# Optimization experiments

Hardware: AMD Instinct MI355X
Metric: run time of the kernel (lower is better)

The kernel has to match this reference:

```python
import jax, jax.numpy as jnp
import numpy as np
from jax import lax

C_DIM = 64
N_HEADS = 8
PATCH = 3
PAD = (PATCH - 1) // 2
EPS = 1e-6


def _unfold(x, p, pad):
    # x: [B,C,H,W] -> [B, C*p*p, H*W], torch.F.unfold ordering (C slowest, then ph, pw)
    B, C, H, W = x.shape
    xp = jnp.pad(x, ((0, 0), (0, 0), (pad, pad), (pad, pad)))
    cols = jnp.stack([xp[:, :, i:i + H, j:j + W] for i in range(p) for j in range(p)], axis=2)
    return cols.reshape(B, C * p * p, H * W)


def _fold(cols, p, pad, H, W):
    # cols: [B, C*p*p, H*W] -> [B,C,H,W] via col2im scatter-add (torch.F.fold)
    B = cols.shape[0]
    C = cols.shape[1] // (p * p)
    cols = cols.reshape(B, C, p * p, H, W)
    out = jnp.zeros((B, C, H + 2 * pad, W + 2 * pad), cols.dtype)
    for i in range(p):
        for j in range(p):
            out = out.at[:, :, i:i + H, j:j + W].add(cols[:, :, i * p + j])
    return out[:, :, pad:pad + H, pad:pad + W]


def _linear_attn(q, k, v):
    # q,k,v: [B, h, N, d]; non-softmax linear attention with ReLU features
    kv = jnp.einsum('bhnd,bhne->bhde', k, v)          # [B,h,d,d]
    ksum = k.sum(axis=2)                              # [B,h,d]
    denom = jnp.einsum('bhnd,bhd->bhn', q, ksum) + EPS
    out = jnp.einsum('bhnd,bhde->bhne', q, kv) / denom[..., None]
    return out


def setup_inputs() -> dict:
    key = jax.random.key(0)
    ks = jax.random.split(key, 5)
    B, C, H, W = 4, C_DIM, 128, 128
    x = jax.random.normal(ks[0], (B, C, H, W), jnp.float32)
    w_qkv = jax.random.normal(ks[1], (3 * C, C), jnp.float32) * 0.05
    b_qkv = jax.random.normal(ks[2], (3 * C,), jnp.float32) * 0.01
    w_proj = jax.random.normal(ks[3], (C, C, 3, 3), jnp.float32) * 0.05
    b_proj = jax.random.normal(ks[4], (C,), jnp.float32) * 0.01
    return {"x": x, "w_qkv": w_qkv, "b_qkv": b_qkv, "w_proj": w_proj, "b_proj": b_proj}


def reference(x, w_qkv, b_qkv, w_proj, b_proj):
    B, C, H, W = x.shape
    p, pad, h = PATCH, PAD, N_HEADS
    N = H * W
    # 1x1 conv qkv
    qkv = jnp.einsum('bchw,oc->bohw', x, w_qkv) + b_qkv[None, :, None, None]
    q, k, v = qkv[:, :C], qkv[:, C:2 * C], qkv[:, 2 * C:]
    q = jax.nn.relu(q)
    k = jax.nn.relu(k)
    # im2col: [B, C*p*p, N]
    qc = _unfold(q, p, pad)
    kc = _unfold(k, p, pad)
    vc = _unfold(v, p, pad)
    d = (C * p * p) // h
    qh = qc.reshape(B, h, d, N).transpose(0, 1, 3, 2)  # [B,h,N,d]
    kh = kc.reshape(B, h, d, N).transpose(0, 1, 3, 2)
    vh = vc.reshape(B, h, d, N).transpose(0, 1, 3, 2)
    o = _linear_attn(qh, kh, vh)                       # [B,h,N,d]
    oc = o.transpose(0, 1, 3, 2).reshape(B, C * p * p, N)
    folded = _fold(oc, p, pad, H, W)
    ones_cols = _unfold(jnp.ones((B, C, H, W), x.dtype), p, pad)
    counts = _fold(ones_cols, p, pad, H, W)
    y = folded / counts
    # 3x3 proj conv
    y = lax.conv_general_dilated(y, w_proj, (1, 1), [(1, 1), (1, 1)],
                                 dimension_numbers=('NCHW', 'OIHW', 'NCHW'))
    y = y + b_proj[None, :, None, None]
    return y
```

## Files before the change

### kernel.cpp

```cpp
#include <hip/hip_runtime.h>

#define BB 4
#define CC 64
#define HH 128
#define WW 128
#define NN (HH*WW)
#define HP 130
#define NPP (HP*HP)
#define HPS 136
#define VROWS 132
#define NPPS (VROWS*HPS)
#define HP2 132
#define NPP2 (HP2*HP2)
#define NH 8
#define DD 72

__global__ __launch_bounds__(256) void kz_pads(float* __restrict__ Qp, float* __restrict__ Kp,
                                               float* __restrict__ rfp){
    const int t = threadIdx.x;
    const int c = blockIdx.x;
    if (c < 256){
        float* f = Qp + (size_t)c*NPP2;
        for (int idx=t; idx<4*HP2; idx+=256){
            int rs = idx / HP2, col = idx - rs*HP2;
            int row = (rs<2)? rs : (128+rs);
            f[row*HP2 + col] = 0.f;
        }
        for (int idx=t; idx<128*4; idx+=256){
            int row = 2 + (idx>>2), cs = idx&3;
            int col = (cs<2)? cs : (128+cs);
            f[row*HP2 + col] = 0.f;
        }
    } else if (c < 768){
        float* f = Kp + (size_t)(c-256)*NPPS;
        for (int idx=t; idx<4*HPS; idx+=256){
            int rs = idx / HPS, col = idx - rs*HPS;
            int row = (rs<2)? rs : (128+rs);
            f[row*HPS + col] = 0.f;
        }
        for (int idx=t; idx<128*8; idx+=256){
            int row = 2 + (idx>>3), cs = idx&7;
            int col = (cs<4)? cs : (128+cs);
            f[row*HPS + col] = 0.f;
        }
    } else {
        float* f = rfp + (size_t)(c-768)*NPP;
        for (int idx=t; idx<2*HP; idx+=256){
            int rs = idx / HP, col = idx - rs*HP;
            f[(rs?129:0)*HP + col] = 0.f;
        }
        for (int idx=t; idx<128*2; idx+=256){
            int row = 1 + (idx>>1);
            f[row*HP + ((idx&1)?129:0)] = 0.f;
        }
    }
}

__global__ __launch_bounds__(256) void k0_wt(const float* __restrict__ wproj,
                                             const float* __restrict__ wqkv,
                                             float* __restrict__ wt, float* __restrict__ wqkvT){
    int idx = blockIdx.x*256 + threadIdx.x;
    if (idx < 64*9*64){
        int oc = idx & 63;
        int w  = (idx >> 6) % 9;
        int ci = idx / 576;
        wt[idx] = wproj[(oc*64 + ci)*9 + w];
    } else if (idx < 64*9*64 + 3*64*64){
        int i2 = idx - 64*9*64;
        int orel = i2 & 63, c = (i2 >> 6) & 63, gy = i2 >> 12;
        wqkvT[i2] = wqkv[(gy*64 + orel)*64 + c];
    }
}

__global__ __launch_bounds__(256) void k1_qkv(const float* __restrict__ x,
        const float* __restrict__ wqkvT, const float* __restrict__ bqkv,
        float* __restrict__ Qp, float* __restrict__ Kp, float* __restrict__ Vp){
    const int t = threadIdx.x;
    const int gy = blockIdx.y;
    const int b  = blockIdx.z;
    const int pix = blockIdx.x*256 + t;
    float acc[64];
#pragma unroll
    for (int o=0;o<64;++o) acc[o]=0.f;
    const float* xb = x + (size_t)(b*64)*NN + pix;
    const float* wT = wqkvT + gy*4096;
    for (int c=0;c<64;++c){
        float xv = xb[(size_t)c*NN];
        const float4* wr = (const float4*)(wT + c*64);
#pragma unroll
        for (int o4=0;o4<16;++o4){
            float4 wv = wr[o4];
            acc[o4*4+0] += xv*wv.x;
            acc[o4*4+1] += xv*wv.y;
            acc[o4*4+2] += xv*wv.z;
            acc[o4*4+3] += xv*wv.w;
        }
    }
    const int y = pix >> 7, xx = pix & 127;
    float* dst; size_t cstride;
    if (gy == 0){ dst = Qp + (size_t)(b*64)*NPP2 + (y+2)*HP2 + (xx+2); cstride = NPP2; }
    else { dst = ((gy==1)?Kp:Vp) + (size_t)(b*64)*NPPS + (y+2)*HPS + (xx+4); cstride = NPPS; }
    const bool dorelu = (gy < 2);
    const float* bl = bqkv + gy*64;
#pragma unroll
    for (int o=0;o<64;++o){
        float v = acc[o] + bl[o];
        if (dorelu) v = fmaxf(v, 0.f);
        dst[(size_t)o*cstride] = v;
    }
}

__global__ __launch_bounds__(256) void k2_ksum(const float* __restrict__ Kp, float* __restrict__ ksum){
    const int c = blockIdx.x, b = blockIdx.y;
    const float* src = Kp + (size_t)(b*64 + c)*NPPS;
    float a[3][3];
#pragma unroll
    for (int i=0;i<3;++i)
#pragma unroll
        for (int j=0;j<3;++j) a[i][j]=0.f;
    for (int idx = threadIdx.x; idx < NPPS; idx += 256){
        int r = idx / HPS, cc = idx - r*HPS;
        float v = src[idx];
#pragma unroll
        for (int i=0;i<3;++i){
            bool fy = (unsigned)(r - 1 - i) < 128u;
#pragma unroll
            for (int j=0;j<3;++j){
                bool fx = (unsigned)(cc - 3 - j) < 128u;
                if (fy && fx) a[i][j] += v;
            }
        }
    }
    __shared__ float red[4][9];
#pragma unroll
    for (int i=0;i<3;++i)
#pragma unroll
        for (int j=0;j<3;++j){
            float v = a[i][j];
            for (int m=1;m<64;m<<=1) v += __shfl_xor(v, m, 64);
            a[i][j] = v;
        }
    int wave = threadIdx.x >> 6, lane = threadIdx.x & 63;
    if (lane == 0){
#pragma unroll
        for (int w=0;w<9;++w) red[wave][w] = a[w/3][w%3];
    }
    __syncthreads();
    if (threadIdx.x < 9){
        float s = red[0][threadIdx.x]+red[1][threadIdx.x]+red[2][threadIdx.x]+red[3][threadIdx.x];
        int h = c >> 3, cl = c & 7;
        ksum[(b*NH + h)*DD + cl*9 + threadIdx.x] = s;
    }
}

__global__ __launch_bounds__(256) void k3a_corr(const float* __restrict__ Kp, const float* __restrict__ Vp,
                                                float* __restrict__ Cpart){
    const int t = threadIdx.x;
    const int pair = blockIdx.x;
    const int cd = pair >> 3, ce = pair & 7;
    const int h = blockIdx.y, b = blockIdx.z;
    const int bh = b*NH + h;
    const float* Kc = Kp + (size_t)(b*64 + h*8 + cd)*NPPS;
    const float* Vc = Vp + (size_t)(b*64 + h*8 + ce)*NPPS;
    const int x0 = (t & 31) * 4;
    const int yb = t >> 5;
    const int y0 = yb*16;
    float C[25];
#pragma unroll
    for (int k=0;k<25;++k) C[k]=0.f;

    float vv[5][12];
    const float* vbase = Vc + (size_t)y0*HPS + x0;
#pragma unroll
    for (int rr=0; rr<4; ++rr){
#pragma unroll
        for (int q=0;q<3;++q){
            float4 a = *(const float4*)(vbase + rr*HPS + 4*q);
            vv[rr][4*q]=a.x; vv[rr][4*q+1]=a.y; vv[rr][4*q+2]=a.z; vv[rr][4*q+3]=a.w;
        }
    }
#pragma unroll
    for (int it=0; it<16; ++it){
        const int slot = (it+4)%5;
#pragma unroll
        for (int q=0;q<3;++q){
            float4 a = *(const float4*)(vbase + (it+4)*HPS + 4*q);
            vv[slot][4*q]=a.x; vv[slot][4*q+1]=a.y; vv[slot][4*q+2]=a.z; vv[slot][4*q+3]=a.w;
        }
        float4 kk4 = *(const float4*)(Kc + (size_t)(y0+it+2)*HPS + 4 + x0);
        float kk[4] = {kk4.x, kk4.y, kk4.z, kk4.w};
#pragma unroll
        for (int dr=0; dr<5; ++dr){
            const float* vrow = vv[(it+dr)%5];
#pragma unroll
            for (int dj=0; dj<5; ++dj)
#pragma unroll
                for (int p=0; p<4; ++p)
                    C[dr*5+dj] += kk[p] * vrow[p+dj+2];
        }
    }
#pragma unroll
    for (int k=0;k<25;++k){
        float v = C[k];
        for (int m=1;m<64;m<<=1) v += __shfl_xor(v, m, 64);
        C[k] = v;
    }
    __shared__ float red[4][25];
    const int wave = t >> 6, lane = t & 63;
    if (lane == 0){
#pragma unroll
        for (int k=0;k<25;++k) red[wave][k] = C[k];
    }
    __syncthreads();
    if (t < 25){
        float s = red[0][t]+red[1][t]+red[2][t]+red[3][t];
        Cpart[((size_t)bh*64 + pair)*25 + t] = s;
    }
}

__global__ __launch_bounds__(128) void k3c_kv(const float* __restrict__ Kp, const float* __restrict__ Vp,
                                              const float* __restrict__ Cpart, float* __restrict__ kvT2){
    __shared__ float Krow[2][136];
    __shared__ float Vrow[10][136];
    __shared__ float Kcol[132][2];
    __shared__ float Vcol[132][16];
    __shared__ float corr[100];
    __shared__ float C25s[25];
    const int t = threadIdx.x;
    const int pair = blockIdx.x;
    const int cd = pair >> 3, ce = pair & 7;
    const int h = blockIdx.y, b = blockIdx.z;
    const int bh = b*NH + h;
    const float* Kc = Kp + (size_t)(b*64 + h*8 + cd)*NPPS;
    const float* Vc = Vp + (size_t)(b*64 + h*8 + ce)*NPPS;
    for (int idx=t; idx<2*136; idx+=128){
        int side = idx/136, col = idx - side*136;
        Krow[side][col] = Kc[(side?129:2)*HPS + col];
    }
    for (int idx=t; idx<10*136; idx+=128){
        int s = idx/136, col = idx - s*136;
        int row = (s<5)? s : (122+s);
        Vrow[s][col] = Vc[row*HPS + col];
    }
    for (int idx=t; idx<132*2; idx+=128){
        int row = idx>>1, side = idx&1;
        Kcol[row][side] = Kc[row*HPS + (side?131:4)];
    }
    for (int idx=t; idx<132*16; idx+=128){
        int row = idx>>4, g = idx&15;
        Vcol[row][g] = Vc[row*HPS + ((g<8)? g : (120+g))];
    }
    __syncthreads();
    if (t < 100){
        int kind = t/50, rem = t%50, side = rem/25, sh = rem%25;
        int di2 = sh/5, dj2 = sh - di2*5;
        float s = 0.f;
        if (kind == 0){
            const float* kr = &Krow[side][4];
            const float* vr = &Vrow[side*5+di2][2+dj2];
            for (int bb=0; bb<128; ++bb) s += kr[bb]*vr[bb];
        } else {
            const int g = side? (9+dj2) : (2+dj2);
            for (int a=0; a<128; ++a) s += Kcol[2+a][side]*Vcol[a+di2][g];
        }
        corr[t] = s;
    } else if (t < 125){
        C25s[t-100] = Cpart[((size_t)bh*64 + pair)*25 + (t-100)];
    }
    __syncthreads();
    if (t < 81){
        int i = t/27, j = (t/9)%3, i2 = (t/3)%3, j2 = t%3;
        int di2 = i2-i+2, dj2 = j2-j+2;
        float val = C25s[di2*5+dj2];
        int si = (i==0)?1:0;
        int sj = (j==0)?1:0;
        if (i != 1) val -= corr[si*25 + di2*5 + dj2];
        if (j != 1) val -= corr[50 + sj*25 + di2*5 + dj2];
        if (i != 1 && j != 1){
            int cj = (j==0)?127:0;
            val += Krow[si][4+cj] * Vrow[si*5+di2][2+cj+dj2];
        }
        kvT2[((size_t)bh*DD + ce*9 + i2*3 + j2)*96 + cd*12 + i*3 + j] = val;
    }
}

__global__ __launch_bounds__(256) void k4_r(const float* __restrict__ Qp, const float* __restrict__ ksum,
                                            float* __restrict__ rfp){
    const int h = blockIdx.y, b = blockIdx.z;
    __shared__ float ks[72];
    if (threadIdx.x < 72) ks[threadIdx.x] = ksum[(b*NH + h)*DD + threadIdx.x];
    __syncthreads();
    const int pix = blockIdx.x*256 + threadIdx.x;
    const int y = pix >> 7, xx = pix & 127;
    const float* Qb = Qp + (size_t)(b*64 + h*8)*NPP2 + (y+1)*HP2 + (xx+1);
    float denom = 0.f;
#pragma unroll
    for (int cl=0; cl<8; ++cl){
        const float* q = Qb + (size_t)cl*NPP2;
#pragma unroll
        for (int w=0; w<9; ++w){
            denom += q[(w/3)*HP2 + (w%3)] * ks[cl*9 + w];
        }
    }
    rfp[(size_t)(b*NH + h)*NPP + (y+1)*HP + (xx+1)] = 1.f/(denom + 1e-6f);
}

__global__ __launch_bounds__(512) void k5_attn(const float* __restrict__ Qp, const float* __restrict__ kvT2,
          const float* __restrict__ rfp, float* __restrict__ folded){
    __shared__ __align__(16) float Qt[8*20*20];
    __shared__ __align__(16) float rt[18*20];
    const int t = threadIdx.x;
    const int tile = blockIdx.x;
    const int h = blockIdx.y, b = blockIdx.z;
    const int ty0 = (tile >> 3)*16, tx0 = (tile & 7)*16;

    const float* Qb = Qp + (size_t)(b*64 + h*8)*NPP2 + (size_t)ty0*HP2 + tx0;
    for (int idx=t; idx<8*20*20; idx+=512){
        int cl = idx / 400; int rem = idx - cl*400; int r = rem/20, cc = rem - r*20;
        Qt[idx] = Qb[(size_t)cl*NPP2 + r*HP2 + cc];
    }
    const float* rg = rfp + (size_t)(b*NH + h)*NPP + (size_t)ty0*HP + tx0;
    for (int idx=t; idx<18*18; idx+=512){
        int rr = idx / 18, cc = idx - rr*18;
        rt[rr*20 + cc] = rg[rr*HP + cc];
    }
    __syncthreads();

    const int c  = __builtin_amdgcn_readfirstlane(t >> 6);
    const int l  = t & 63;
    const int pr = l >> 2;
    const int pc = (l & 3) * 4;

    const float* kvc = kvT2 + ((size_t)(b*NH + h)*DD + c*9)*96;

    float acc[9][4];
#pragma unroll
    for (int u=0;u<9;++u)
#pragma unroll
        for (int p=0;p<4;++p) acc[u][p]=0.f;

    for (int cl=0; cl<8; ++cl){
        float qw[5][8];
        const float* qb = &Qt[cl*400 + pr*20 + pc];
#pragma unroll
        for (int rr=0; rr<5; ++rr){
            float4 a0 = *(const float4*)(qb + rr*20);
            float4 a1 = *(const float4*)(qb + rr*20 + 4);
            qw[rr][0]=a0.x; qw[rr][1]=a0.y; qw[rr][2]=a0.z; qw[rr][3]=a0.w;
            qw[rr][4]=a1.x; qw[rr][5]=a1.y; qw[rr][6]=a1.z; qw[rr][7]=a1.w;
        }
#pragma unroll
        for (int u=0; u<9; ++u){
            const float* kr = kvc + u*96 + cl*12;
            float kw[9];
#pragma unroll
            for (int i=0;i<9;++i) kw[i] = kr[i];
            const int iu = u/3, ju = u - iu*3;
#pragma unroll
            for (int w=0; w<9; ++w){
                const int rr = (w/3) - iu + 2;
                const int cc = (w%3) - ju + 2;
#pragma unroll
                for (int p=0;p<4;++p)
                    acc[u][p] += qw[rr][cc+p] * kw[w];
            }
        }
    }
    float rw[3][6];
    const float* rb = &rt[pr*20 + pc];
#pragma unroll
    for (int rr=0; rr<3; ++rr)
#pragma unroll
        for (int j=0; j<6; ++j) rw[rr][j] = rb[rr*20 + j];
    float out[4];
#pragma unroll
    for (int p=0;p<4;++p) out[p]=0.f;
#pragma unroll
    for (int u=0; u<9; ++u){
        const int iu = u/3, ju = u - iu*3;
#pragma unroll
        for (int p=0;p<4;++p)
            out[p] += acc[u][p] * rw[2-iu][p+2-ju];
    }
    const int iy = ty0 + pr;
    const float ry = 3.f - (float)(iy==0) - (float)(iy==127);
#pragma unroll
    for (int p=0;p<4;++p){
        const int ix = tx0 + pc + p;
        const float rx = 3.f - (float)(ix==0) - (float)(ix==127);
        out[p] = out[p] / (ry*rx);
    }
    float4 o4 = make_float4(out[0], out[1], out[2], out[3]);
    *(float4*)(&folded[(size_t)(b*64 + h*8 + c)*NN + (ty0+pr)*WW + tx0 + pc]) = o4;
}

__global__ __launch_bounds__(256) void k6_conv(const float* __restrict__ folded, const float* __restrict__ wt,
         const float* __restrict__ bproj, float* __restrict__ out){
    __shared__ __align__(16) float ut[64*18*12];
    const int t = threadIdx.x;
    const int tile = blockIdx.x;
    const int b = blockIdx.y;
    const int ty0 = (tile >> 4)*16, tx0 = (tile & 15)*8;

    for (int idx=t; idx<64*18*10; idx+=256){
        int ci = idx / 180; int rem = idx - ci*180; int rr = rem/10, cc = rem - rr*10;
        int iy = ty0 - 1 + rr, ix = tx0 - 1 + cc;
        float v = 0.f;
        if ((unsigned)iy < 128u && (unsigned)ix < 128u)
            v = folded[(size_t)(b*64 + ci)*NN + iy*WW + ix];
        ut[ci*216 + rr*12 + cc] = v;
    }
    __syncthreads();

    const int ocq = t & 15;
    const int s   = t >> 4;
    float acc[4][8];
#pragma unroll
    for (int ol=0;ol<4;++ol)
#pragma unroll
        for (int p=0;p<8;++p) acc[ol][p]=0.f;

    for (int ci=0; ci<64; ++ci){
        float uw[3][10];
        const float* ub = &ut[ci*216 + s*12];
#pragma unroll
        for (int dy=0;dy<3;++dy){
            float4 a0 = *(const float4*)(ub + dy*12);
            float4 a1 = *(const float4*)(ub + dy*12 + 4);
            float2 a2 = *(const float2*)(ub + dy*12 + 8);
            uw[dy][0]=a0.x; uw[dy][1]=a0.y; uw[dy][2]=a0.z; uw[dy][3]=a0.w;
            uw[dy][4]=a1.x; uw[dy][5]=a1.y; uw[dy][6]=a1.z; uw[dy][7]=a1.w;
            uw[dy][8]=a2.x; uw[dy][9]=a2.y;
        }
#pragma unroll
        for (int w=0;w<9;++w){
            const int dy = w/3, dx = w%3;
            float4 wv = *(const float4*)(&wt[(ci*9 + w)*64 + ocq*4]);
#pragma unroll
            for (int p=0;p<8;++p){
                float u = uw[dy][p+dx];
                acc[0][p] += wv.x*u;
                acc[1][p] += wv.y*u;
                acc[2][p] += wv.z*u;
                acc[3][p] += wv.w*u;
            }
        }
    }
    const int y = ty0 + s;
    const float4 bias = *(const float4*)(&bproj[ocq*4]);
#pragma unroll
    for (int ol=0;ol<4;++ol){
        const int oc = ocq*4 + ol;
        float* dst = &out[(size_t)(b*64 + oc)*NN + y*WW + tx0];
        const float bv = (ol==0)?bias.x:(ol==1)?bias.y:(ol==2)?bias.z:bias.w;
        float4 v0 = make_float4(acc[ol][0]+bv, acc[ol][1]+bv, acc[ol][2]+bv, acc[ol][3]+bv);
        float4 v1 = make_float4(acc[ol][4]+bv, acc[ol][5]+bv, acc[ol][6]+bv, acc[ol][7]+bv);
        *(float4*)(dst)     = v0;
        *(float4*)(dst + 4) = v1;
    }
}

extern "C" void kernel_launch(void* const* d_in, const int* in_sizes, int n_in,
                              void* d_out, int out_size, void* d_ws, size_t ws_size,
                              hipStream_t stream) {
    const float* x     = (const float*)d_in[0];
    const float* wqkv  = (const float*)d_in[1];
    const float* bqkv  = (const float*)d_in[2];
    const float* wproj = (const float*)d_in[3];
    const float* bproj = (const float*)d_in[4];
    float* out = (float*)d_out;
    float* ws  = (float*)d_ws;

    const size_t szQ2 = (size_t)BB*CC*NPP2;
    const size_t szFS = (size_t)BB*CC*NPPS;
    const size_t szR  = (size_t)BB*NH*NPP;
    const size_t szKV = (size_t)BB*NH*DD*96;
    const size_t szKS = (size_t)BB*NH*DD;
    float* Qp2    = ws;
    float* Kp     = Qp2 + szQ2;
    float* Vp     = Kp + szFS;
    float* rfp    = Vp + szFS;
    float* kvT2   = rfp + szR;
    float* ksum   = kvT2 + szKV;
    float* folded = ksum + szKS;
    float* wt     = folded + (size_t)BB*CC*NN;
    float* wqkvT  = wt + (size_t)64*9*64;
    float* Cpart  = folded;

    kz_pads <<<dim3(800),      256, 0, stream>>>(Qp2, Kp, rfp);
    k0_wt   <<<dim3(192),      256, 0, stream>>>(wproj, wqkv, wt, wqkvT);
    k1_qkv  <<<dim3(64, 3, 4), 256, 0, stream>>>(x, wqkvT, bqkv, Qp2, Kp, Vp);
    k2_ksum <<<dim3(64, 4),    256, 0, stream>>>(Kp, ksum);
    k3a_corr<<<dim3(64, 8, 4), 256, 0, stream>>>(Kp, Vp, Cpart);
    k3c_kv  <<<dim3(64, 8, 4), 128, 0, stream>>>(Kp, Vp, Cpart, kvT2);
    k4_r    <<<dim3(64, 8, 4), 256, 0, stream>>>(Qp2, ksum, rfp);
    k5_attn <<<dim3(64, 8, 4), 512, 0, stream>>>(Qp2, kvT2, rfp, folded);
    k6_conv <<<dim3(128, 4),   256, 0, stream>>>(folded, wt, bproj, out);
}
```

Before: 346.6 us.

## Retile 3x3 projection conv: 8x8 spatial tiles, wave-uniform output channels

The 3x3 projection convolution now uses 8x8 spatial tiles instead of 16x8, doubling the grid to 1024 blocks for better occupancy across compute units. Each wave owns 16 output channels, read through a wave-uniform index, so weight loads can become scalar broadcasts. Each lane computes one pixel for those 16 channels. Register blocking drops from 4x8 to 16x1, so each thread does fewer FMAs per shared-memory load, and more halo data is reloaded relative to tile size.

```diff
diff --git a/kernel.cpp b/kernel.cpp
--- a/kernel.cpp
+++ b/kernel.cpp
@@ -396,68 +396,53 @@
 
 __global__ __launch_bounds__(256) void k6_conv(const float* __restrict__ folded, const float* __restrict__ wt,
          const float* __restrict__ bproj, float* __restrict__ out){
-    __shared__ __align__(16) float ut[64*18*12];
+    __shared__ float ut[64*120];
     const int t = threadIdx.x;
     const int tile = blockIdx.x;
     const int b = blockIdx.y;
-    const int ty0 = (tile >> 4)*16, tx0 = (tile & 15)*8;
-
-    for (int idx=t; idx<64*18*10; idx+=256){
-        int ci = idx / 180; int rem = idx - ci*180; int rr = rem/10, cc = rem - rr*10;
+    const int ty0 = (tile >> 4)*8, tx0 = (tile & 15)*8;
+
+    for (int idx=t; idx<6400; idx+=256){
+        int ci = idx / 100; int rem = idx - ci*100; int rr = rem/10, cc = rem - rr*10;
         int iy = ty0 - 1 + rr, ix = tx0 - 1 + cc;
         float v = 0.f;
         if ((unsigned)iy < 128u && (unsigned)ix < 128u)
             v = folded[(size_t)(b*64 + ci)*NN + iy*WW + ix];
-        ut[ci*216 + rr*12 + cc] = v;
-    }
-    __syncthreads();
-
-    const int ocq = t & 15;
-    const int s   = t >> 4;
-    float acc[4][8];
-#pragma unroll
-    for (int ol=0;ol<4;++ol)
-#pragma unroll
-        for (int p=0;p<8;++p) acc[ol][p]=0.f;
-
+        ut[ci*120 + rr*12 + cc] = v;
+    }
+    __syncthreads();
+
+    const int wv4 = __builtin_amdgcn_readfirstlane(t >> 6);
+    const int ocb = wv4*16;
+    const int l  = t & 63;
+    const int pr = l >> 3, pc = l & 7;
+
+    float acc[16];
+#pragma unroll
+    for (int o=0;o<16;++o) acc[o]=0.f;
+
+    const float* ub0 = &ut[pr*12 + pc];
+    const float* wb  = wt + ocb;
     for (int ci=0; ci<64; ++ci){
-        float uw[3][10];
-        const float* ub = &ut[ci*216 + s*12];
-#pragma unroll
-        for (int dy=0;dy<3;++dy){
-            float4 a0 = *(const float4*)(ub + dy*12);
-            float4 a1 = *(const float4*)(ub + dy*12 + 4);
-            float2 a2 = *(const float2*)(ub + dy*12 + 8);
-            uw[dy][0]=a0.x; uw[dy][1]=a0.y; uw[dy][2]=a0.z; uw[dy][3]=a0.w;
-            uw[dy][4]=a1.x; uw[dy][5]=a1.y; uw[dy][6]=a1.z; uw[dy][7]=a1.w;
-            uw[dy][8]=a2.x; uw[dy][9]=a2.y;
-        }
+        float u[9];
+        const float* uc = ub0 + ci*120;
+#pragma unroll
+        for (int dy=0;dy<3;++dy)
+#pragma unroll
+            for (int dx=0;dx<3;++dx) u[dy*3+dx] = uc[dy*12 + dx];
 #pragma unroll
         for (int w=0;w<9;++w){
-            const int dy = w/3, dx = w%3;
-            float4 wv = *(const float4*)(&wt[(ci*9 + w)*64 + ocq*4]);
-#pragma unroll
-            for (int p=0;p<8;++p){
-                float u = uw[dy][p+dx];
-                acc[0][p] += wv.x*u;
-                acc[1][p] += wv.y*u;
-                acc[2][p] += wv.z*u;
-                acc[3][p] += wv.w*u;
-            }
-        }
-    }
-    const int y = ty0 + s;
-    const float4 bias = *(const float4*)(&bproj[ocq*4]);
-#pragma unroll
-    for (int ol=0;ol<4;++ol){
-        const int oc = ocq*4 + ol;
-        float* dst = &out[(size_t)(b*64 + oc)*NN + y*WW + tx0];
-        const float bv = (ol==0)?bias.x:(ol==1)?bias.y:(ol==2)?bias.z:bias.w;
-        float4 v0 = make_float4(acc[ol][0]+bv, acc[ol][1]+bv, acc[ol][2]+bv, acc[ol][3]+bv);
-        float4 v1 = make_float4(acc[ol][4]+bv, acc[ol][5]+bv, acc[ol][6]+bv, acc[ol][7]+bv);
-        *(float4*)(dst)     = v0;
-        *(float4*)(dst + 4) = v1;
-    }
+            const float* kr = wb + (ci*9 + w)*64;
+            const float uv = u[w];
+#pragma unroll
+            for (int o=0;o<16;++o) acc[o] += kr[o]*uv;
+        }
+    }
+    const int y = ty0 + pr, x = tx0 + pc;
+    const float* bb = bproj + ocb;
+    float* dst = &out[(size_t)(b*64 + ocb)*NN + y*WW + x];
+#pragma unroll
+    for (int o=0;o<16;++o) dst[(size_t)o*NN] = acc[o] + bb[o];
 }
 
 extern "C" void kernel_launch(void* const* d_in, const int* in_sizes, int n_in,
@@ -495,5 +480,5 @@
     k3c_kv  <<<dim3(64, 8, 4), 128, 0, stream>>>(Kp, Vp, Cpart, kvT2);
     k4_r    <<<dim3(64, 8, 4), 256, 0, stream>>>(Qp2, ksum, rfp);
     k5_attn <<<dim3(64, 8, 4), 512, 0, stream>>>(Qp2, kvT2, rfp, folded);
-    k6_conv <<<dim3(128, 4),   256, 0, stream>>>(folded, wt, bproj, out);
-}
+    k6_conv <<<dim3(256, 4),   256, 0, stream>>>(folded, wt, bproj, out);
+}
```

Result: no change. 345.4 us (-0.3%).
